# Optimization experiments

Measured on AMD Instinct MI355X. Metric: run time of the kernel, lower is better.

## Reference

```python
import jax, jax.numpy as jnp
import numpy as np

B, D, C = 512, 512, 85742   # batch, in_features, out_features (MS1M identities)
M = 4                       # angular margin order -> cos(4*theta) = 8c^4 - 8c^2 + 1
PI = 3.14159265             # constant used in the torch source
LAMB = max(5.0, 1000.0 * (1.0 + 0.12 * 1) ** -1.0)  # lamb at iter=1 (first forward)
EPS = 1e-12                 # torch F.normalize eps


def setup_inputs() -> dict:
    key = jax.random.key(0)
    k1, k2, k3 = jax.random.split(key, 3)
    x = jax.random.normal(k1, (B, D), dtype=jnp.float32)
    label = jax.random.randint(k2, (B,), 0, C)
    limit = np.sqrt(6.0 / (D + C))  # xavier_uniform bound for weight [C, D]
    weight = jax.random.uniform(k3, (C, D), minval=-limit, maxval=limit, dtype=jnp.float32)
    return {"x": x, "weight": weight, "label": label}


def reference(x, weight, label):
    # row-normalize features and class weights (F.normalize, p=2, dim=1)
    xn = x / jnp.maximum(jnp.linalg.norm(x, axis=1, keepdims=True), EPS)
    wn = weight / jnp.maximum(jnp.linalg.norm(weight, axis=1, keepdims=True), EPS)
    cos = jnp.clip(xn @ wn.T, -1.0, 1.0)                       # [B, C] cosine logits
    cos_m = 8.0 * cos**4 - 8.0 * cos**2 + 1.0                  # cos(4*theta), m=4
    # theta/k computed on detached cos (torch uses cos_theta.data)
    theta = jnp.arccos(jax.lax.stop_gradient(cos))
    k = jnp.floor(M * theta / PI)
    phi = (-1.0) ** k * cos_m - 2.0 * k                        # [B, C]
    feat_norm = jnp.linalg.norm(x, axis=1)                     # [B]
    one_hot = jax.nn.one_hot(label, C, dtype=cos.dtype)        # scatter of 1s at label
    out = (one_hot * (phi - cos) / (1.0 + LAMB) + cos) * feat_norm[:, None]
    # cross-entropy, mean reduction
    logp = jax.nn.log_softmax(out, axis=1)
    loss = -jnp.take_along_axis(logp, label[:, None], axis=1).mean()
    return loss
```

## Files before the change

kernel.cpp:

```cpp
#include <hip/hip_runtime.h>
#include <stdint.h>

#define D_K 512
#define C_CLS 85742
#define N_TILES 670
#define N_PART (N_TILES * 2)

using bf16x8 = __attribute__((ext_vector_type(8))) short;
using f32x4  = __attribute__((ext_vector_type(4))) float;

__device__ __forceinline__ unsigned int cvtpk(float a, float b) {
  unsigned int r;
  asm("v_cvt_pk_bf16_f32 %0, %1, %2" : "=v"(r) : "v"(a), "v"(b));
  return r;
}
__device__ __forceinline__ unsigned short f2bf(float f) {
  unsigned int u = __builtin_bit_cast(unsigned int, f);
  u += 0x7FFFu + ((u >> 16) & 1u);
  return (unsigned short)(u >> 16);
}
__device__ __forceinline__ float bf2f(unsigned short h) {
  return __builtin_bit_cast(float, ((unsigned int)h) << 16);
}
__device__ __forceinline__ float sq8(const float4& a, const float4& b) {
  return a.x*a.x + a.y*a.y + a.z*a.z + a.w*a.w +
         b.x*b.x + b.y*b.y + b.z*b.z + b.w*b.w;
}

__global__ __launch_bounds__(256) void k_xnorm(const float* __restrict__ X,
                                               unsigned short* __restrict__ XN,
                                               float* __restrict__ FN) {
  int row  = blockIdx.x * 4 + (threadIdx.x >> 6);
  int lane = threadIdx.x & 63;
  const float4* px = (const float4*)(X + (size_t)row * D_K + lane * 8);
  float4 u = px[0], v = px[1];
  float nsq = sq8(u, v);
#pragma unroll
  for (int m = 1; m <= 32; m <<= 1) nsq += __shfl_xor(nsq, m);
  float nrm = sqrtf(nsq);
  float inv = 1.0f / fmaxf(nrm, 1e-12f);
  uint4 o;
  o.x = cvtpk(u.x*inv, u.y*inv); o.y = cvtpk(u.z*inv, u.w*inv);
  o.z = cvtpk(v.x*inv, v.y*inv); o.w = cvtpk(v.z*inv, v.w*inv);
  *(uint4*)(XN + (size_t)row * D_K + lane * 8) = o;
  if (lane == 0) FN[row] = nrm;
}

__global__ __launch_bounds__(256) void k_gemm_lse(const float* __restrict__ W,
                                                  const unsigned short* __restrict__ XN,
                                                  const float* __restrict__ FN,
                                                  float2* __restrict__ PART) {
  __shared__ alignas(16) unsigned short As[2][4096];
  __shared__ alignas(16) unsigned short Bs[2][4096];
  __shared__ float nsqS[128];
  __shared__ float fnS[128];

  int bid = blockIdx.x;
  int wg    = (bid & 7) * 335 + (bid >> 3);
  int ntile = wg >> 2, mtile = wg & 3;
  int m0 = mtile * 128, n0 = ntile * 128;

  int t    = threadIdx.x;
  int lane = t & 63, wid = t >> 6;
  int wm = wid >> 1, wn = wid & 1;
  int s = lane & 15, g = lane >> 4;

  int r1 = t >> 2;
  int c0 = (t & 3) * 8;
  int gr1 = n0 + r1;      if (gr1 > C_CLS - 1) gr1 = C_CLS - 1;
  int gr2 = n0 + 64 + r1; if (gr2 > C_CLS - 1) gr2 = C_CLS - 1;
  const float* pB1 = W + (size_t)gr1 * D_K + c0;
  const float* pB2 = W + (size_t)gr2 * D_K + c0;

  const unsigned short* gA0 = XN + (size_t)(m0 + wid * 16 + (lane >> 2)) * D_K + (lane & 3) * 8;
  f32x4 acc[4][4] = {};
  float nsq1 = 0.f, nsq2 = 0.f;
  float4 ra0, ra1, rb0, rb1;

#define GLDS(srcp, dstp) __builtin_amdgcn_global_load_lds( \
    (const __attribute__((address_space(1))) unsigned int*)(srcp), \
    (__attribute__((address_space(3))) unsigned int*)(dstp), 16, 0, 0)

#define STAGE_A(b, kk) do { \
    GLDS(gA0 + (size_t)(kk) * 32,            &As[b][wid * 512]); \
    GLDS(gA0 + 64 * D_K + (size_t)(kk) * 32, &As[b][2048 + wid * 512]); \
  } while (0)

#define PREF_B(kk) do { \
    const float* q1_ = pB1 + (size_t)(kk) * 32; \
    const float* q2_ = pB2 + (size_t)(kk) * 32; \
    ra0 = *(const float4*)q1_; ra1 = *(const float4*)(q1_ + 4); \
    rb0 = *(const float4*)q2_; rb1 = *(const float4*)(q2_ + 4); \
  } while (0)

#define CONV_B(b) do { \
    nsq1 += sq8(ra0, ra1); \
    nsq2 += sq8(rb0, rb1); \
    uint4 u1_, u2_; \
    u1_.x = cvtpk(ra0.x, ra0.y); u1_.y = cvtpk(ra0.z, ra0.w); \
    u1_.z = cvtpk(ra1.x, ra1.y); u1_.w = cvtpk(ra1.z, ra1.w); \
    u2_.x = cvtpk(rb0.x, rb0.y); u2_.y = cvtpk(rb0.z, rb0.w); \
    u2_.z = cvtpk(rb1.x, rb1.y); u2_.w = cvtpk(rb1.z, rb1.w); \
    *(uint4*)(&Bs[b][t * 8])        = u1_; \
    *(uint4*)(&Bs[b][2048 + t * 8]) = u2_; \
  } while (0)

#define FRAGS_MFMA(b) do { \
    bf16x8 af[4], bfr[4]; \
    _Pragma("unroll") for (int mf = 0; mf < 4; ++mf) \
      af[mf] = *(const bf16x8*)(&As[b][(wm * 64 + mf * 16 + s) * 32 + g * 8]); \
    _Pragma("unroll") for (int nf = 0; nf < 4; ++nf) \
      bfr[nf] = *(const bf16x8*)(&Bs[b][(wn * 64 + nf * 16 + s) * 32 + g * 8]); \
    _Pragma("unroll") for (int mf = 0; mf < 4; ++mf) \
      _Pragma("unroll") for (int nf = 0; nf < 4; ++nf) \
        acc[mf][nf] = __builtin_amdgcn_mfma_f32_16x16x32_bf16(af[mf], bfr[nf], acc[mf][nf], 0, 0, 0); \
  } while (0)

  STAGE_A(0, 0);
  PREF_B(0);
  if (t < 128) fnS[t] = FN[m0 + t];
  CONV_B(0);
  __syncthreads();

  for (int kt = 0; kt < 15; ++kt) {
    int cur = kt & 1;
    STAGE_A(cur ^ 1, kt + 1);
    PREF_B(kt + 1);
    FRAGS_MFMA(cur);
    CONV_B(cur ^ 1);
    __syncthreads();
  }
  FRAGS_MFMA(1);

  nsq1 += __shfl_xor(nsq1, 1); nsq1 += __shfl_xor(nsq1, 2);
  nsq2 += __shfl_xor(nsq2, 1); nsq2 += __shfl_xor(nsq2, 2);
  if ((t & 3) == 0) { nsqS[r1] = nsq1; nsqS[64 + r1] = nsq2; }
  __syncthreads();

  float rinv[4]; int cvalid[4];
#pragma unroll
  for (int nf = 0; nf < 4; ++nf) {
    int cl = wn * 64 + nf * 16 + s;
    cvalid[nf] = (n0 + cl) < C_CLS;
    rinv[nf] = 1.0f / fmaxf(sqrtf(nsqS[cl]), 1e-12f);
  }
  const float NEG_INF = -__builtin_inff();
#pragma unroll
  for (int mf = 0; mf < 4; ++mf) {
#pragma unroll
    for (int q = 0; q < 4; ++q) {
      int rl = wm * 64 + mf * 16 + g * 4 + q;
      float fr = fnS[rl];
      float z[4]; float mx = NEG_INF;
#pragma unroll
      for (int nf = 0; nf < 4; ++nf) {
        float cc = acc[mf][nf][q] * rinv[nf];
        cc = fminf(fmaxf(cc, -1.0f), 1.0f);
        z[nf] = cvalid[nf] ? cc * fr : NEG_INF;
        mx = fmaxf(mx, z[nf]);
      }
#pragma unroll
      for (int d = 1; d <= 8; d <<= 1) mx = fmaxf(mx, __shfl_xor(mx, d));
      float se = 0.f;
#pragma unroll
      for (int nf = 0; nf < 4; ++nf) se += __expf(z[nf] - mx);
#pragma unroll
      for (int d = 1; d <= 8; d <<= 1) se += __shfl_xor(se, d);
      if (s == mf * 4 + q)
        PART[(size_t)(m0 + rl) * N_PART + (ntile * 2 + wn)] = make_float2(mx, se);
    }
  }
}

__global__ __launch_bounds__(64) void k_target(const float* __restrict__ W,
                                               const unsigned short* __restrict__ XN,
                                               const float* __restrict__ FN,
                                               const int* __restrict__ LBL,
                                               float2* __restrict__ ZT) {
  int row = blockIdx.x;
  int lane = threadIdx.x;
  int lab = LBL[row];
  const float* pw = W + (size_t)lab * D_K + lane * 8;
  const unsigned short* px = XN + (size_t)row * D_K + lane * 8;
  float dot = 0.f, nsq = 0.f;
#pragma unroll
  for (int j = 0; j < 8; ++j) {
    float w = pw[j];
    nsq += w * w;
    dot += bf2f(px[j]) * bf2f(f2bf(w));
  }
#pragma unroll
  for (int m = 1; m <= 32; m <<= 1) { dot += __shfl_xor(dot, m); nsq += __shfl_xor(nsq, m); }
  if (lane == 0) {
    const float LAMB = 1000.0f / 1.12f;
    float rinv = 1.0f / fmaxf(sqrtf(nsq), 1e-12f);
    float c = fminf(fmaxf(dot * rinv, -1.0f), 1.0f);
    float c2 = c * c;
    float cm = 8.0f * c2 * c2 - 8.0f * c2 + 1.0f;
    float th = acosf(c);
    float kf = floorf(4.0f * th / 3.14159265f);
    float phi = ((((int)kf) & 1) ? -cm : cm) - 2.0f * kf;
    float fr = FN[row];
    float zu = fr * c;
    float zm = fr * (c + (phi - c) / (1.0f + LAMB));
    ZT[row] = make_float2(zu, zm);
  }
}

__global__ __launch_bounds__(256) void k_lse(const float2* __restrict__ PART,
                                             const float2* __restrict__ ZT,
                                             float* __restrict__ LOSSI) {
  int row = blockIdx.x;
  int t = threadIdx.x;
  const float NEG_INF = -__builtin_inff();
  float m = NEG_INF, ss = 0.f;
  for (int p = t; p < N_PART; p += 256) {
    float2 ps = PART[(size_t)row * N_PART + p];
    if (ps.y > 0.f) {
      if (ps.x > m) { ss = ss * __expf(m - ps.x) + ps.y; m = ps.x; }
      else          { ss += ps.y * __expf(ps.x - m); }
    }
  }
  __shared__ float sm[256], sv[256];
  sm[t] = m; sv[t] = ss;
  __syncthreads();
  for (int o = 128; o > 0; o >>= 1) {
    if (t < o) {
      float m1 = sm[t], s1 = sv[t];
      float m2 = sm[t + o], s2 = sv[t + o];
      float mm = fmaxf(m1, m2);
      float e1 = (m1 > NEG_INF) ? s1 * __expf(m1 - mm) : 0.f;
      float e2 = (m2 > NEG_INF) ? s2 * __expf(m2 - mm) : 0.f;
      sm[t] = mm; sv[t] = e1 + e2;
    }
    __syncthreads();
  }
  if (t == 0) {
    float M = sm[0], S = sv[0];
    float2 zt = ZT[row];
    S += __expf(zt.y - M) - __expf(zt.x - M);
    LOSSI[row] = M + logf(S) - zt.y;
  }
}

__global__ __launch_bounds__(256) void k_mean(const float* __restrict__ LOSSI,
                                              float* __restrict__ OUT) {
  int t = threadIdx.x;
  float s_ = LOSSI[t] + LOSSI[t + 256];
#pragma unroll
  for (int m = 1; m <= 32; m <<= 1) s_ += __shfl_xor(s_, m);
  __shared__ float wsum[4];
  if ((t & 63) == 0) wsum[t >> 6] = s_;
  __syncthreads();
  if (t == 0) OUT[0] = (wsum[0] + wsum[1] + wsum[2] + wsum[3]) * (1.0f / 512.0f);
}

extern "C" void kernel_launch(void* const* d_in, const int* in_sizes, int n_in,
                              void* d_out, int out_size, void* d_ws, size_t ws_size,
                              hipStream_t stream) {
  const float* X   = (const float*)d_in[0];
  const float* W   = (const float*)d_in[1];
  const int*   LBL = (const int*)d_in[2];
  float* OUT = (float*)d_out;

  char* ws = (char*)d_ws;
  unsigned short* XN = (unsigned short*)ws;
  float*  FN    = (float*)(ws + 524288);
  float2* ZT    = (float2*)(ws + 526336);
  float*  LOSSI = (float*)(ws + 530432);
  float2* PART  = (float2*)(ws + 532480);

  k_xnorm  <<<dim3(128),  dim3(256), 0, stream>>>(X, XN, FN);
  k_gemm_lse<<<dim3(2680), dim3(256), 0, stream>>>(W, XN, FN, PART);
  k_target <<<dim3(512),  dim3(64),  0, stream>>>(W, XN, FN, LBL, ZT);
  k_lse    <<<dim3(512),  dim3(256), 0, stream>>>(PART, ZT, LOSSI);
  k_mean   <<<dim3(1),    dim3(256), 0, stream>>>(LOSSI, OUT);
}
```

Before: 112.6 us.

## Enlarge GEMM tile to 256x128 with 512-thread blocks to halve weight reloads

Each workgroup now covers 256 batch rows instead of 128, using 8 waves. Every fp32 weight tile is therefore loaded, converted to bf16 and norm-accumulated by 2 workgroups instead of 4, which is meant to cut global weight traffic and redundant conversion work. The grid shrinks to 1344 blocks with 672 padded n-tiles, and the k-loop is manually unrolled by two so the double-buffer indices are constants. The trade-offs are larger LDS use per block, occupancy pinned by launch_bounds(512,2), and a less even tail across CUs.

```diff
diff --git a/kernel.cpp b/kernel.cpp
--- a/kernel.cpp
+++ b/kernel.cpp
@@ -3,7 +3,7 @@
 
 #define D_K 512
 #define C_CLS 85742
-#define N_TILES 670
+#define N_TILES 672
 #define N_PART (N_TILES * 2)
 
 using bf16x8 = __attribute__((ext_vector_type(8))) short;
@@ -46,63 +46,54 @@
   if (lane == 0) FN[row] = nrm;
 }
 
-__global__ __launch_bounds__(256) void k_gemm_lse(const float* __restrict__ W,
-                                                  const unsigned short* __restrict__ XN,
-                                                  const float* __restrict__ FN,
-                                                  float2* __restrict__ PART) {
-  __shared__ alignas(16) unsigned short As[2][4096];
+__global__ __launch_bounds__(512, 2) void k_gemm_lse(const float* __restrict__ W,
+                                                     const unsigned short* __restrict__ XN,
+                                                     const float* __restrict__ FN,
+                                                     float2* __restrict__ PART) {
+  __shared__ alignas(16) unsigned short As[2][8192];
   __shared__ alignas(16) unsigned short Bs[2][4096];
   __shared__ float nsqS[128];
-  __shared__ float fnS[128];
+  __shared__ float fnS[256];
 
   int bid = blockIdx.x;
-  int wg    = (bid & 7) * 335 + (bid >> 3);
-  int ntile = wg >> 2, mtile = wg & 3;
-  int m0 = mtile * 128, n0 = ntile * 128;
+  int wg    = (bid & 7) * 168 + (bid >> 3);
+  int ntile = wg >> 1, mtile = wg & 1;
+  int m0 = mtile * 256, n0 = ntile * 128;
 
   int t    = threadIdx.x;
   int lane = t & 63, wid = t >> 6;
   int wm = wid >> 1, wn = wid & 1;
   int s = lane & 15, g = lane >> 4;
 
-  int r1 = t >> 2;
-  int c0 = (t & 3) * 8;
-  int gr1 = n0 + r1;      if (gr1 > C_CLS - 1) gr1 = C_CLS - 1;
-  int gr2 = n0 + 64 + r1; if (gr2 > C_CLS - 1) gr2 = C_CLS - 1;
-  const float* pB1 = W + (size_t)gr1 * D_K + c0;
-  const float* pB2 = W + (size_t)gr2 * D_K + c0;
-
-  const unsigned short* gA0 = XN + (size_t)(m0 + wid * 16 + (lane >> 2)) * D_K + (lane & 3) * 8;
+  int rB = t >> 2;
+  int gr = n0 + rB; if (gr > C_CLS - 1) gr = C_CLS - 1;
+  const float* pB = W + (size_t)gr * D_K + (t & 3) * 8;
+
+  const unsigned short* gA0 = XN + (size_t)(m0 + wid * 32 + (lane >> 2)) * D_K + (lane & 3) * 8;
   f32x4 acc[4][4] = {};
-  float nsq1 = 0.f, nsq2 = 0.f;
-  float4 ra0, ra1, rb0, rb1;
+  float nsq = 0.f;
+  float4 ra0, ra1;
 
 #define GLDS(srcp, dstp) __builtin_amdgcn_global_load_lds( \
     (const __attribute__((address_space(1))) unsigned int*)(srcp), \
     (__attribute__((address_space(3))) unsigned int*)(dstp), 16, 0, 0)
 
 #define STAGE_A(b, kk) do { \
-    GLDS(gA0 + (size_t)(kk) * 32,            &As[b][wid * 512]); \
-    GLDS(gA0 + 64 * D_K + (size_t)(kk) * 32, &As[b][2048 + wid * 512]); \
+    GLDS(gA0 + (size_t)(kk) * 32,            &As[b][wid * 1024]); \
+    GLDS(gA0 + 16 * D_K + (size_t)(kk) * 32, &As[b][wid * 1024 + 512]); \
   } while (0)
 
 #define PREF_B(kk) do { \
-    const float* q1_ = pB1 + (size_t)(kk) * 32; \
-    const float* q2_ = pB2 + (size_t)(kk) * 32; \
-    ra0 = *(const float4*)q1_; ra1 = *(const float4*)(q1_ + 4); \
-    rb0 = *(const float4*)q2_; rb1 = *(const float4*)(q2_ + 4); \
+    const float* q_ = pB + (size_t)(kk) * 32; \
+    ra0 = *(const float4*)q_; ra1 = *(const float4*)(q_ + 4); \
   } while (0)
 
 #define CONV_B(b) do { \
-    nsq1 += sq8(ra0, ra1); \
-    nsq2 += sq8(rb0, rb1); \
-    uint4 u1_, u2_; \
-    u1_.x = cvtpk(ra0.x, ra0.y); u1_.y = cvtpk(ra0.z, ra0.w); \
-    u1_.z = cvtpk(ra1.x, ra1.y); u1_.w = cvtpk(ra1.z, ra1.w); \
-    u2_.x = cvtpk(rb0.x, rb0.y); u2_.y = cvtpk(rb0.z, rb0.w); \
-    u2_.z = cvtpk(rb1.x, rb1.y); u2_.w = cvtpk(rb1.z, rb1.w); \
-    *(uint4*)(&Bs[b][t * 8])        = u1_; \
-    *(uint4*)(&Bs[b][2048 + t * 8]) = u2_; \
+    nsq += sq8(ra0, ra1); \
+    uint4 u_; \
+    u_.x = cvtpk(ra0.x, ra0.y); u_.y = cvtpk(ra0.z, ra0.w); \
+    u_.z = cvtpk(ra1.x, ra1.y); u_.w = cvtpk(ra1.z, ra1.w); \
+    *(uint4*)(&Bs[b][rB * 32 + (t & 3) * 8]) = u_; \
   } while (0)
 
 #define FRAGS_MFMA(b) do { \
@@ -118,23 +109,31 @@
 
   STAGE_A(0, 0);
   PREF_B(0);
-  if (t < 128) fnS[t] = FN[m0 + t];
+  if (t < 256) fnS[t] = FN[m0 + t];
   CONV_B(0);
   __syncthreads();
 
-  for (int kt = 0; kt < 15; ++kt) {
-    int cur = kt & 1;
-    STAGE_A(cur ^ 1, kt + 1);
+  for (int kt = 0; kt < 14; kt += 2) {
+    STAGE_A(1, kt + 1);
     PREF_B(kt + 1);
-    FRAGS_MFMA(cur);
-    CONV_B(cur ^ 1);
+    FRAGS_MFMA(0);
+    CONV_B(1);
     __syncthreads();
-  }
+    STAGE_A(0, kt + 2);
+    PREF_B(kt + 2);
+    FRAGS_MFMA(1);
+    CONV_B(0);
+    __syncthreads();
+  }
+  STAGE_A(1, 15);
+  PREF_B(15);
+  FRAGS_MFMA(0);
+  CONV_B(1);
+  __syncthreads();
   FRAGS_MFMA(1);
 
-  nsq1 += __shfl_xor(nsq1, 1); nsq1 += __shfl_xor(nsq1, 2);
-  nsq2 += __shfl_xor(nsq2, 1); nsq2 += __shfl_xor(nsq2, 2);
-  if ((t & 3) == 0) { nsqS[r1] = nsq1; nsqS[64 + r1] = nsq2; }
+  nsq += __shfl_xor(nsq, 1); nsq += __shfl_xor(nsq, 2);
+  if ((t & 3) == 0) nsqS[rB] = nsq;
   __syncthreads();
 
   float rinv[4]; int cvalid[4];
@@ -271,7 +270,7 @@
   float2* PART  = (float2*)(ws + 532480);
 
   k_xnorm  <<<dim3(128),  dim3(256), 0, stream>>>(X, XN, FN);
-  k_gemm_lse<<<dim3(2680), dim3(256), 0, stream>>>(W, XN, FN, PART);
+  k_gemm_lse<<<dim3(1344), dim3(512), 0, stream>>>(W, XN, FN, PART);
   k_target <<<dim3(512),  dim3(64),  0, stream>>>(W, XN, FN, LBL, ZT);
   k_lse    <<<dim3(512),  dim3(256), 0, stream>>>(PART, ZT, LOSSI);
   k_mean   <<<dim3(1),    dim3(256), 0, stream>>>(LOSSI, OUT);
```

After: 151.1 us. +34.2%, slower.

## Stream fp32 W tiles straight to LDS with a triple-buffered async pipeline

Applied to the files above, without the earlier changes.

W is now staged into LDS as fp32 through global_load_lds, with an XOR swizzle against bank conflicts. The bf16 conversion and the row-norm accumulation move into the fragment-load step, so the register prefetch and conversion stage is gone. The kernel uses three LDS buffers with a prefetch distance of two and waits on vmcnt instead of fully draining at each barrier. This costs more LDS (about 72KB), which may lower occupancy. Each wave also redoes the conversion and norm work for its own fragments, and FN is read from global memory in the epilogue.

```diff
diff --git a/kernel.cpp b/kernel.cpp
--- a/kernel.cpp
+++ b/kernel.cpp
@@ -50,10 +50,8 @@
                                                   const unsigned short* __restrict__ XN,
                                                   const float* __restrict__ FN,
                                                   float2* __restrict__ PART) {
-  __shared__ alignas(16) unsigned short As[2][4096];
-  __shared__ alignas(16) unsigned short Bs[2][4096];
-  __shared__ float nsqS[128];
-  __shared__ float fnS[128];
+  __shared__ alignas(16) unsigned short As[3][4096];
+  __shared__ alignas(16) float          Bs[3][4096];
 
   int bid = blockIdx.x;
   int wg    = (bid & 7) * 335 + (bid >> 3);
@@ -65,84 +63,93 @@
   int wm = wid >> 1, wn = wid & 1;
   int s = lane & 15, g = lane >> 4;
 
-  int r1 = t >> 2;
-  int c0 = (t & 3) * 8;
-  int gr1 = n0 + r1;      if (gr1 > C_CLS - 1) gr1 = C_CLS - 1;
-  int gr2 = n0 + 64 + r1; if (gr2 > C_CLS - 1) gr2 = C_CLS - 1;
-  const float* pB1 = W + (size_t)gr1 * D_K + c0;
-  const float* pB2 = W + (size_t)gr2 * D_K + c0;
-
   const unsigned short* gA0 = XN + (size_t)(m0 + wid * 16 + (lane >> 2)) * D_K + (lane & 3) * 8;
+
+  const float* pB0; const float* pB1; const float* pB2; const float* pB3;
+  {
+#define BSRC(j, dst) do { \
+    int c_ = ((wid * 4 + (j)) * 64) + lane; \
+    int r_ = c_ >> 3, k_ = c_ & 7; \
+    int kl_ = k_ ^ (r_ & 7); \
+    int gr_ = n0 + r_; if (gr_ > C_CLS - 1) gr_ = C_CLS - 1; \
+    dst = W + (size_t)gr_ * D_K + kl_ * 4; \
+  } while (0)
+    BSRC(0, pB0); BSRC(1, pB1); BSRC(2, pB2); BSRC(3, pB3);
+#undef BSRC
+  }
+
   f32x4 acc[4][4] = {};
-  float nsq1 = 0.f, nsq2 = 0.f;
-  float4 ra0, ra1, rb0, rb1;
+  float nsq[4] = {0.f, 0.f, 0.f, 0.f};
 
 #define GLDS(srcp, dstp) __builtin_amdgcn_global_load_lds( \
     (const __attribute__((address_space(1))) unsigned int*)(srcp), \
     (__attribute__((address_space(3))) unsigned int*)(dstp), 16, 0, 0)
 
-#define STAGE_A(b, kk) do { \
+#define STAGE(b, kk) do { \
     GLDS(gA0 + (size_t)(kk) * 32,            &As[b][wid * 512]); \
     GLDS(gA0 + 64 * D_K + (size_t)(kk) * 32, &As[b][2048 + wid * 512]); \
-  } while (0)
-
-#define PREF_B(kk) do { \
-    const float* q1_ = pB1 + (size_t)(kk) * 32; \
-    const float* q2_ = pB2 + (size_t)(kk) * 32; \
-    ra0 = *(const float4*)q1_; ra1 = *(const float4*)(q1_ + 4); \
-    rb0 = *(const float4*)q2_; rb1 = *(const float4*)(q2_ + 4); \
-  } while (0)
-
-#define CONV_B(b) do { \
-    nsq1 += sq8(ra0, ra1); \
-    nsq2 += sq8(rb0, rb1); \
-    uint4 u1_, u2_; \
-    u1_.x = cvtpk(ra0.x, ra0.y); u1_.y = cvtpk(ra0.z, ra0.w); \
-    u1_.z = cvtpk(ra1.x, ra1.y); u1_.w = cvtpk(ra1.z, ra1.w); \
-    u2_.x = cvtpk(rb0.x, rb0.y); u2_.y = cvtpk(rb0.z, rb0.w); \
-    u2_.z = cvtpk(rb1.x, rb1.y); u2_.w = cvtpk(rb1.z, rb1.w); \
-    *(uint4*)(&Bs[b][t * 8])        = u1_; \
-    *(uint4*)(&Bs[b][2048 + t * 8]) = u2_; \
+    GLDS(pB0 + (size_t)(kk) * 32, &Bs[b][(wid * 4 + 0) * 256]); \
+    GLDS(pB1 + (size_t)(kk) * 32, &Bs[b][(wid * 4 + 1) * 256]); \
+    GLDS(pB2 + (size_t)(kk) * 32, &Bs[b][(wid * 4 + 2) * 256]); \
+    GLDS(pB3 + (size_t)(kk) * 32, &Bs[b][(wid * 4 + 3) * 256]); \
   } while (0)
 
 #define FRAGS_MFMA(b) do { \
     bf16x8 af[4], bfr[4]; \
     _Pragma("unroll") for (int mf = 0; mf < 4; ++mf) \
       af[mf] = *(const bf16x8*)(&As[b][(wm * 64 + mf * 16 + s) * 32 + g * 8]); \
-    _Pragma("unroll") for (int nf = 0; nf < 4; ++nf) \
-      bfr[nf] = *(const bf16x8*)(&Bs[b][(wn * 64 + nf * 16 + s) * 32 + g * 8]); \
+    _Pragma("unroll") for (int nf = 0; nf < 4; ++nf) { \
+      int R_ = wn * 64 + nf * 16 + s; \
+      int p0_ = (2 * g) ^ (R_ & 7); \
+      const float4* q0_ = (const float4*)(&Bs[b][R_ * 32 + p0_ * 4]); \
+      const float4* q1_ = (const float4*)(&Bs[b][R_ * 32 + (p0_ ^ 1) * 4]); \
+      float4 w0_ = *q0_, w1_ = *q1_; \
+      nsq[nf] += sq8(w0_, w1_); \
+      uint4 u_; \
+      u_.x = cvtpk(w0_.x, w0_.y); u_.y = cvtpk(w0_.z, w0_.w); \
+      u_.z = cvtpk(w1_.x, w1_.y); u_.w = cvtpk(w1_.z, w1_.w); \
+      bfr[nf] = __builtin_bit_cast(bf16x8, u_); \
+    } \
     _Pragma("unroll") for (int mf = 0; mf < 4; ++mf) \
       _Pragma("unroll") for (int nf = 0; nf < 4; ++nf) \
         acc[mf][nf] = __builtin_amdgcn_mfma_f32_16x16x32_bf16(af[mf], bfr[nf], acc[mf][nf], 0, 0, 0); \
   } while (0)
 
-  STAGE_A(0, 0);
-  PREF_B(0);
-  if (t < 128) fnS[t] = FN[m0 + t];
-  CONV_B(0);
-  __syncthreads();
-
-  for (int kt = 0; kt < 15; ++kt) {
-    int cur = kt & 1;
-    STAGE_A(cur ^ 1, kt + 1);
-    PREF_B(kt + 1);
+#define BARC() do { \
+    asm volatile("s_waitcnt vmcnt(6) lgkmcnt(0)" ::: "memory"); \
+    __builtin_amdgcn_s_barrier(); } while (0)
+#define BAR0() do { \
+    asm volatile("s_waitcnt vmcnt(0) lgkmcnt(0)" ::: "memory"); \
+    __builtin_amdgcn_s_barrier(); } while (0)
+
+  STAGE(0, 0);
+  STAGE(1, 1);
+  BARC();
+
+  for (int kt = 0; kt < 13; ++kt) {
+    int cur = kt % 3;
+    int nxt = (kt + 2) % 3;
+    STAGE(nxt, kt + 2);
     FRAGS_MFMA(cur);
-    CONV_B(cur ^ 1);
-    __syncthreads();
-  }
+    BARC();
+  }
+  STAGE(0, 15);
   FRAGS_MFMA(1);
-
-  nsq1 += __shfl_xor(nsq1, 1); nsq1 += __shfl_xor(nsq1, 2);
-  nsq2 += __shfl_xor(nsq2, 1); nsq2 += __shfl_xor(nsq2, 2);
-  if ((t & 3) == 0) { nsqS[r1] = nsq1; nsqS[64 + r1] = nsq2; }
-  __syncthreads();
-
+  BARC();
+  FRAGS_MFMA(2);
+  BAR0();
+  FRAGS_MFMA(0);
+
+#pragma unroll
+  for (int nf = 0; nf < 4; ++nf) {
+    nsq[nf] += __shfl_xor(nsq[nf], 16);
+    nsq[nf] += __shfl_xor(nsq[nf], 32);
+  }
   float rinv[4]; int cvalid[4];
 #pragma unroll
   for (int nf = 0; nf < 4; ++nf) {
-    int cl = wn * 64 + nf * 16 + s;
-    cvalid[nf] = (n0 + cl) < C_CLS;
-    rinv[nf] = 1.0f / fmaxf(sqrtf(nsqS[cl]), 1e-12f);
+    cvalid[nf] = (n0 + wn * 64 + nf * 16 + s) < C_CLS;
+    rinv[nf] = 1.0f / fmaxf(sqrtf(nsq[nf]), 1e-12f);
   }
   const float NEG_INF = -__builtin_inff();
 #pragma unroll
@@ -150,7 +157,7 @@
 #pragma unroll
     for (int q = 0; q < 4; ++q) {
       int rl = wm * 64 + mf * 16 + g * 4 + q;
-      float fr = fnS[rl];
+      float fr = FN[m0 + rl];
       float z[4]; float mx = NEG_INF;
 #pragma unroll
       for (int nf = 0; nf < 4; ++nf) {
```

Result: slower. 168.1 us (+49.3%).

## Precompute bf16 weights and inverse norms in a separate pass before GEMM

Applied to the files above, without the earlier changes.

Adds a k_wnorm pre-pass that converts the fp32 weight matrix to bf16 and stores per-class inverse norms in workspace. The GEMM then loads both operands with direct global-to-LDS loads instead of converting fp32 in registers. This is meant to remove the repeated fp32 weight reads and conversion work across the four M-tiles. In exchange it adds an extra kernel that reads the full weight matrix and writes about 88 MB. A fallback to the old kernel is kept for when the workspace is too small.

```diff
diff --git a/kernel.cpp b/kernel.cpp
--- a/kernel.cpp
+++ b/kernel.cpp
@@ -26,6 +26,10 @@
   return a.x*a.x + a.y*a.y + a.z*a.z + a.w*a.w +
          b.x*b.x + b.y*b.y + b.z*b.z + b.w*b.w;
 }
+
+#define GLDS(srcp, dstp) __builtin_amdgcn_global_load_lds( \
+    (const __attribute__((address_space(1))) unsigned int*)(srcp), \
+    (__attribute__((address_space(3))) unsigned int*)(dstp), 16, 0, 0)
 
 __global__ __launch_bounds__(256) void k_xnorm(const float* __restrict__ X,
                                                unsigned short* __restrict__ XN,
@@ -46,10 +50,117 @@
   if (lane == 0) FN[row] = nrm;
 }
 
-__global__ __launch_bounds__(256) void k_gemm_lse(const float* __restrict__ W,
-                                                  const unsigned short* __restrict__ XN,
-                                                  const float* __restrict__ FN,
-                                                  float2* __restrict__ PART) {
+__global__ __launch_bounds__(256) void k_wnorm(const float* __restrict__ W,
+                                               unsigned short* __restrict__ WBF,
+                                               float* __restrict__ RINV) {
+  int row  = blockIdx.x * 4 + (threadIdx.x >> 6);
+  if (row >= C_CLS) return;
+  int lane = threadIdx.x & 63;
+  const float4* pw = (const float4*)(W + (size_t)row * D_K + lane * 8);
+  float4 u = pw[0], v = pw[1];
+  float nsq = sq8(u, v);
+#pragma unroll
+  for (int m = 1; m <= 32; m <<= 1) nsq += __shfl_xor(nsq, m);
+  uint4 o;
+  o.x = cvtpk(u.x, u.y); o.y = cvtpk(u.z, u.w);
+  o.z = cvtpk(v.x, v.y); o.w = cvtpk(v.z, v.w);
+  *(uint4*)(WBF + (size_t)row * D_K + lane * 8) = o;
+  if (lane == 0) RINV[row] = 1.0f / fmaxf(sqrtf(nsq), 1e-12f);
+}
+
+__global__ __launch_bounds__(256) void k_gemm2(const unsigned short* __restrict__ WBF,
+                                               const unsigned short* __restrict__ XN,
+                                               const float* __restrict__ FN,
+                                               const float* __restrict__ RINV,
+                                               float2* __restrict__ PART) {
+  __shared__ alignas(16) unsigned short As[2][4096];
+  __shared__ alignas(16) unsigned short Bs[2][4096];
+
+  int bid = blockIdx.x;
+  int wg    = (bid & 7) * 335 + (bid >> 3);
+  int ntile = wg >> 2, mtile = wg & 3;
+  int m0 = mtile * 128, n0 = ntile * 128;
+
+  int t    = threadIdx.x;
+  int lane = t & 63, wid = t >> 6;
+  int wm = wid >> 1, wn = wid & 1;
+  int s = lane & 15, g = lane >> 4;
+
+  const unsigned short* gA0 = XN + (size_t)(m0 + wid * 16 + (lane >> 2)) * D_K + (lane & 3) * 8;
+  const unsigned short* gA1 = gA0 + (size_t)64 * D_K;
+  int rB0 = n0 + wid * 16 + (lane >> 2); if (rB0 > C_CLS - 1) rB0 = C_CLS - 1;
+  int rB1 = n0 + 64 + wid * 16 + (lane >> 2); if (rB1 > C_CLS - 1) rB1 = C_CLS - 1;
+  const unsigned short* gB0 = WBF + (size_t)rB0 * D_K + (lane & 3) * 8;
+  const unsigned short* gB1 = WBF + (size_t)rB1 * D_K + (lane & 3) * 8;
+
+  f32x4 acc[4][4] = {};
+
+#define STAGE(b, kk) do { \
+    GLDS(gA0 + (size_t)(kk) * 32, &As[b][wid * 512]); \
+    GLDS(gA1 + (size_t)(kk) * 32, &As[b][2048 + wid * 512]); \
+    GLDS(gB0 + (size_t)(kk) * 32, &Bs[b][wid * 512]); \
+    GLDS(gB1 + (size_t)(kk) * 32, &Bs[b][2048 + wid * 512]); \
+  } while (0)
+
+#define FRAGS_MFMA(b) do { \
+    bf16x8 af[4], bfr[4]; \
+    _Pragma("unroll") for (int mf = 0; mf < 4; ++mf) \
+      af[mf] = *(const bf16x8*)(&As[b][(wm * 64 + mf * 16 + s) * 32 + g * 8]); \
+    _Pragma("unroll") for (int nf = 0; nf < 4; ++nf) \
+      bfr[nf] = *(const bf16x8*)(&Bs[b][(wn * 64 + nf * 16 + s) * 32 + g * 8]); \
+    _Pragma("unroll") for (int mf = 0; mf < 4; ++mf) \
+      _Pragma("unroll") for (int nf = 0; nf < 4; ++nf) \
+        acc[mf][nf] = __builtin_amdgcn_mfma_f32_16x16x32_bf16(af[mf], bfr[nf], acc[mf][nf], 0, 0, 0); \
+  } while (0)
+
+  STAGE(0, 0);
+  __syncthreads();
+  for (int kt = 0; kt < 16; ++kt) {
+    int cur = kt & 1;
+    if (kt < 15) STAGE(cur ^ 1, kt + 1);
+    FRAGS_MFMA(cur);
+    if (kt < 15) __syncthreads();
+  }
+
+  float rinv[4]; int cvalid[4];
+#pragma unroll
+  for (int nf = 0; nf < 4; ++nf) {
+    int gc = n0 + wn * 64 + nf * 16 + s;
+    cvalid[nf] = gc < C_CLS;
+    rinv[nf] = RINV[cvalid[nf] ? gc : C_CLS - 1];
+  }
+  const float NEG_INF = -__builtin_inff();
+#pragma unroll
+  for (int mf = 0; mf < 4; ++mf) {
+#pragma unroll
+    for (int q = 0; q < 4; ++q) {
+      int rl = wm * 64 + mf * 16 + g * 4 + q;
+      float fr = FN[m0 + rl];
+      float z[4]; float mx = NEG_INF;
+#pragma unroll
+      for (int nf = 0; nf < 4; ++nf) {
+        float cc = acc[mf][nf][q] * rinv[nf];
+        cc = fminf(fmaxf(cc, -1.0f), 1.0f);
+        z[nf] = cvalid[nf] ? cc * fr : NEG_INF;
+        mx = fmaxf(mx, z[nf]);
+      }
+#pragma unroll
+      for (int d = 1; d <= 8; d <<= 1) mx = fmaxf(mx, __shfl_xor(mx, d));
+      float se = 0.f;
+#pragma unroll
+      for (int nf = 0; nf < 4; ++nf) se += __expf(z[nf] - mx);
+#pragma unroll
+      for (int d = 1; d <= 8; d <<= 1) se += __shfl_xor(se, d);
+      if (s == mf * 4 + q)
+        PART[(size_t)(m0 + rl) * N_PART + (ntile * 2 + wn)] = make_float2(mx, se);
+    }
+  }
+}
+
+__global__ __launch_bounds__(256) void k_gemm_fb(const float* __restrict__ W,
+                                                 const unsigned short* __restrict__ XN,
+                                                 const float* __restrict__ FN,
+                                                 float2* __restrict__ PART) {
   __shared__ alignas(16) unsigned short As[2][4096];
   __shared__ alignas(16) unsigned short Bs[2][4096];
   __shared__ float nsqS[128];
@@ -77,22 +188,16 @@
   float nsq1 = 0.f, nsq2 = 0.f;
   float4 ra0, ra1, rb0, rb1;
 
-#define GLDS(srcp, dstp) __builtin_amdgcn_global_load_lds( \
-    (const __attribute__((address_space(1))) unsigned int*)(srcp), \
-    (__attribute__((address_space(3))) unsigned int*)(dstp), 16, 0, 0)
-
 #define STAGE_A(b, kk) do { \
     GLDS(gA0 + (size_t)(kk) * 32,            &As[b][wid * 512]); \
     GLDS(gA0 + 64 * D_K + (size_t)(kk) * 32, &As[b][2048 + wid * 512]); \
   } while (0)
-
 #define PREF_B(kk) do { \
     const float* q1_ = pB1 + (size_t)(kk) * 32; \
     const float* q2_ = pB2 + (size_t)(kk) * 32; \
     ra0 = *(const float4*)q1_; ra1 = *(const float4*)(q1_ + 4); \
     rb0 = *(const float4*)q2_; rb1 = *(const float4*)(q2_ + 4); \
   } while (0)
-
 #define CONV_B(b) do { \
     nsq1 += sq8(ra0, ra1); \
     nsq2 += sq8(rb0, rb1); \
@@ -105,23 +210,11 @@
     *(uint4*)(&Bs[b][2048 + t * 8]) = u2_; \
   } while (0)
 
-#define FRAGS_MFMA(b) do { \
-    bf16x8 af[4], bfr[4]; \
-    _Pragma("unroll") for (int mf = 0; mf < 4; ++mf) \
-      af[mf] = *(const bf16x8*)(&As[b][(wm * 64 + mf * 16 + s) * 32 + g * 8]); \
-    _Pragma("unroll") for (int nf = 0; nf < 4; ++nf) \
-      bfr[nf] = *(const bf16x8*)(&Bs[b][(wn * 64 + nf * 16 + s) * 32 + g * 8]); \
-    _Pragma("unroll") for (int mf = 0; mf < 4; ++mf) \
-      _Pragma("unroll") for (int nf = 0; nf < 4; ++nf) \
-        acc[mf][nf] = __builtin_amdgcn_mfma_f32_16x16x32_bf16(af[mf], bfr[nf], acc[mf][nf], 0, 0, 0); \
-  } while (0)
-
   STAGE_A(0, 0);
   PREF_B(0);
   if (t < 128) fnS[t] = FN[m0 + t];
   CONV_B(0);
   __syncthreads();
-
   for (int kt = 0; kt < 15; ++kt) {
     int cur = kt & 1;
     STAGE_A(cur ^ 1, kt + 1);
@@ -269,10 +362,18 @@
   float2* ZT    = (float2*)(ws + 526336);
   float*  LOSSI = (float*)(ws + 530432);
   float2* PART  = (float2*)(ws + 532480);
-
-  k_xnorm  <<<dim3(128),  dim3(256), 0, stream>>>(X, XN, FN);
-  k_gemm_lse<<<dim3(2680), dim3(256), 0, stream>>>(W, XN, FN, PART);
-  k_target <<<dim3(512),  dim3(64),  0, stream>>>(W, XN, FN, LBL, ZT);
-  k_lse    <<<dim3(512),  dim3(256), 0, stream>>>(PART, ZT, LOSSI);
-  k_mean   <<<dim3(1),    dim3(256), 0, stream>>>(LOSSI, OUT);
-}
+  unsigned short* WBF = (unsigned short*)(ws + 6021120);
+  float* RINV   = (float*)(ws + 93820928);
+  const size_t NEED = 94163896;
+
+  k_xnorm<<<dim3(128), dim3(256), 0, stream>>>(X, XN, FN);
+  if (ws_size >= NEED) {
+    k_wnorm<<<dim3((C_CLS + 3) / 4), dim3(256), 0, stream>>>(W, WBF, RINV);
+    k_gemm2<<<dim3(2680), dim3(256), 0, stream>>>(WBF, XN, FN, RINV, PART);
+  } else {
+    k_gemm_fb<<<dim3(2680), dim3(256), 0, stream>>>(W, XN, FN, PART);
+  }
+  k_target<<<dim3(512), dim3(64),  0, stream>>>(W, XN, FN, LBL, ZT);
+  k_lse   <<<dim3(512), dim3(256), 0, stream>>>(PART, ZT, LOSSI);
+  k_mean  <<<dim3(1),   dim3(256), 0, stream>>>(LOSSI, OUT);
+}
```

Result: slower. 132.0 us (+17.2%).
